# Kernel optimization log

Measured on AMD Instinct MI355X. Metric: run time of the kernel, lower is better.

## Reference

```python
import jax, jax.numpy as jnp
import numpy as np

ATOL = 1e-06
RTOL = 1e-06

def setup_inputs() -> dict:
    key = jax.random.key(0)
    ks = jax.random.split(key, 8)
    u = lambda k, shape: jax.random.uniform(k, shape, jnp.float32, -0.05, 0.05)
    return {
        "x": jax.random.normal(ks[0], (4096, 32, 32, 3), jnp.float32),
        "W_lstm": u(ks[1], (3, 16)),      # input kernel, gates [i,f,c,o]
        "U_lstm": u(ks[2], (4, 16)),      # recurrent kernel
        "dw_kernel": u(ks[3], (27, 27, 3, 5)),  # depthwise (kh,kw,in_c,mult)
        "pw_kernel": u(ks[4], (15, 4)),   # pointwise
        "conv_bias": u(ks[5], (4,)),
        "W_td": u(ks[6], (4096, 10)),
        "W_sc": u(ks[7], (4096, 10)),
    }

def _lstm_td(x, W, U):
    # TimeDistributed LSTM: x (B,32,32,3) -> treat axis1 as TD batch, axis2 as time
    B = x.shape[0]
    seq = x.reshape(B * 32, 32, 3)          # (N, T, F)
    xs = jnp.transpose(seq, (1, 0, 2))      # (T, N, F)
    N = seq.shape[0]
    h0 = jnp.zeros((N, 4), x.dtype)
    c0 = jnp.zeros((N, 4), x.dtype)

    def step(carry, xt):
        h, c = carry
        z = xt @ W + h @ U                  # (N, 16)
        zi, zf, zc, zo = jnp.split(z, 4, axis=-1)
        i = jax.nn.elu(zi)                  # recurrent_activation='elu'
        f = jax.nn.elu(zf)
        c = f * c + i * jax.nn.softmax(zc, axis=-1)  # activation='softmax'
        o = jax.nn.elu(zo)
        h = o * jax.nn.softmax(c, axis=-1)
        return (h, c), h

    _, hs = jax.lax.scan(step, (h0, c0), xs)        # (T, N, 4)
    return jnp.transpose(hs, (1, 0, 2)).reshape(B, 32, 32, 4)

def _sep_conv(x, dw_kernel, pw_kernel, conv_bias):
    # depthwise: Keras (kh,kw,C,M) -> lax HWIO grouped (kh,kw,1,C*M), channel-major order
    dw = dw_kernel.reshape(27, 27, 1, 15)
    y = jax.lax.conv_general_dilated(
        x, dw, window_strides=(1, 1), padding='SAME',
        feature_group_count=3,
        dimension_numbers=('NHWC', 'HWIO', 'NHWC'))   # (B,32,32,15)
    y = jnp.einsum('bhwc,cf->bhwf', y, pw_kernel) + conv_bias
    return jax.nn.sigmoid(y)                          # (B,32,32,4)

def reference(x, W_lstm, U_lstm, dw_kernel, pw_kernel, conv_bias, W_td, W_sc):
    B = x.shape[0]
    td = _lstm_td(x, W_lstm, U_lstm).reshape(B, -1) @ W_td   # (B,10)
    sc = _sep_conv(x, dw_kernel, pw_kernel, conv_bias).reshape(B, -1) @ W_sc
    diff = jnp.abs(td - sc)
    tol = ATOL + RTOL * jnp.abs(sc)
    return diff <= tol
```

## Files before the change

### kernel.cpp

```cpp
#include <hip/hip_runtime.h>
#include <math.h>

#define TD_OFF 0
#define WTDR_OFF 40960
#define SC_OFF 81920
#define BG_BYTE_OFF 524288

typedef __bf16 bf16x8 __attribute__((ext_vector_type(8)));
typedef float f32x16 __attribute__((ext_vector_type(16)));

union FragU { bf16x8 v; float4 f; };

__device__ __forceinline__ f32x16 mfma16(bf16x8 a, bf16x8 b, f32x16 c) {
    return __builtin_amdgcn_mfma_f32_32x32x16_bf16(a, b, c, 0, 0, 0);
}

__device__ __forceinline__ float eluf(float v) {
    return v > 0.f ? v : __expf(v) - 1.f;
}

__global__ __launch_bounds__(256) void prep(const float* __restrict__ dw,
                                            const float* __restrict__ pw,
                                            const float* __restrict__ Wtd,
                                            float* __restrict__ Wtdr,
                                            unsigned short* __restrict__ Bg) {
    int gid = blockIdx.x * 256 + threadIdx.x;
    if (gid < 40960) {
        int k = gid & 3;
        int r = gid >> 2;
        int row = r & 31; r >>= 5;
        int j = r % 10;
        int tt = r / 10;
        Wtdr[gid] = Wtd[(size_t)(row * 128 + tt * 4 + k) * 10 + j];
        return;
    }
    int g2 = gid - 40960;
    if (g2 >= 162 * 128) return;
    int n = g2 & 127;
    int s = g2 >> 7;
    int half = s & 1;
    int cd = s >> 1;
    int c = cd / 27, d = cd % 27;
    int w = n >> 2, f = n & 3;
    unsigned short* dsth = Bg + (size_t)s * 4096 + n * 16;
    unsigned short* dstl = dsth + 2048;
#pragma unroll
    for (int k = 0; k < 16; k++) {
        int xi = half * 16 + k;
        int dx = xi - w + 13;
        float v = 0.f;
        if (dx >= 0 && dx < 27) {
#pragma unroll
            for (int m = 0; m < 5; m++)
                v = fmaf(dw[((d * 27 + dx) * 3 + c) * 5 + m],
                         pw[(c * 5 + m) * 4 + f], v);
        }
        __bf16 h = (__bf16)v;
        __bf16 l = (__bf16)(v - (float)h);
        dsth[k] = __builtin_bit_cast(unsigned short, h);
        dstl[k] = __builtin_bit_cast(unsigned short, l);
    }
}

#define A_OFF 0
#define ZOFF 49152
#define SRED_OFF 49168
#define LDS_BYTES 49808

__global__ __launch_bounds__(256, 3) void fused(const float* __restrict__ x,
                                                const float* __restrict__ W,
                                                const float* __restrict__ U,
                                                const float* __restrict__ Wtdr,
                                                const unsigned short* __restrict__ Bg,
                                                const float* __restrict__ Wsc,
                                                const float* __restrict__ bias,
                                                float* __restrict__ td_out,
                                                float* __restrict__ sc_out) {
    __shared__ char LDS[LDS_BYTES] __attribute__((aligned(16)));
    int bx = blockIdx.x;
    int rem = bx % 3;
    int q = bx / 3;
    int t = threadIdx.x;

    if (rem == 2) {
        float rW[48], rU[64];
        const float4* W4 = (const float4*)W;
        const float4* U4 = (const float4*)U;
#pragma unroll
        for (int i = 0; i < 12; i++) {
            float4 qv = W4[i];
            rW[i * 4 + 0] = qv.x; rW[i * 4 + 1] = qv.y;
            rW[i * 4 + 2] = qv.z; rW[i * 4 + 3] = qv.w;
        }
#pragma unroll
        for (int i = 0; i < 16; i++) {
            float4 qv = U4[i];
            rU[i * 4 + 0] = qv.x; rU[i * 4 + 1] = qv.y;
            rU[i * 4 + 2] = qv.z; rU[i * 4 + 3] = qv.w;
        }

        int n = q * 256 + t;
        int row = n & 31;
        const float4* xp4 = (const float4*)(x + (size_t)n * 96);

        float h0 = 0, h1 = 0, h2 = 0, h3 = 0;
        float c0 = 0, c1 = 0, c2 = 0, c3 = 0;
        float acc[10];
#pragma unroll
        for (int j = 0; j < 10; j++) acc[j] = 0.f;

        for (int g = 0; g < 8; g++) {
            float4 q0 = xp4[g * 3 + 0], q1 = xp4[g * 3 + 1], q2 = xp4[g * 3 + 2];
            float xr[12] = {q0.x, q0.y, q0.z, q0.w, q1.x, q1.y,
                            q1.z, q1.w, q2.x, q2.y, q2.z, q2.w};
#pragma unroll
            for (int st = 0; st < 4; st++) {
                int tt = g * 4 + st;
                float x0 = xr[st * 3 + 0], x1 = xr[st * 3 + 1], x2 = xr[st * 3 + 2];
                float z[16];
#pragma unroll
                for (int k = 0; k < 16; k++)
                    z[k] = x0 * rW[k] + x1 * rW[16 + k] + x2 * rW[32 + k]
                         + h0 * rU[k] + h1 * rU[16 + k] + h2 * rU[32 + k] + h3 * rU[48 + k];

                float ig0 = eluf(z[0]),  ig1 = eluf(z[1]),  ig2 = eluf(z[2]),  ig3 = eluf(z[3]);
                float fg0 = eluf(z[4]),  fg1 = eluf(z[5]),  fg2 = eluf(z[6]),  fg3 = eluf(z[7]);
                float og0 = eluf(z[12]), og1 = eluf(z[13]), og2 = eluf(z[14]), og3 = eluf(z[15]);

                float zm = fmaxf(fmaxf(z[8], z[9]), fmaxf(z[10], z[11]));
                float e0 = __expf(z[8] - zm), e1 = __expf(z[9] - zm);
                float e2 = __expf(z[10] - zm), e3 = __expf(z[11] - zm);
                float inv = 1.f / (e0 + e1 + e2 + e3);
                c0 = fg0 * c0 + ig0 * (e0 * inv);
                c1 = fg1 * c1 + ig1 * (e1 * inv);
                c2 = fg2 * c2 + ig2 * (e2 * inv);
                c3 = fg3 * c3 + ig3 * (e3 * inv);

                float cm = fmaxf(fmaxf(c0, c1), fmaxf(c2, c3));
                float p0 = __expf(c0 - cm), p1 = __expf(c1 - cm);
                float p2 = __expf(c2 - cm), p3 = __expf(c3 - cm);
                float pinv = 1.f / (p0 + p1 + p2 + p3);
                h0 = og0 * (p0 * pinv); h1 = og1 * (p1 * pinv);
                h2 = og2 * (p2 * pinv); h3 = og3 * (p3 * pinv);

                const float4* wr4 = (const float4*)(Wtdr + (size_t)tt * 1280) + row;
#pragma unroll
                for (int j = 0; j < 10; j++) {
                    float4 qv = wr4[j * 32];
                    acc[j] += h0 * qv.x + h1 * qv.y + h2 * qv.z + h3 * qv.w;
                }
            }
        }

#pragma unroll
        for (int off = 16; off >= 1; off >>= 1) {
#pragma unroll
            for (int j = 0; j < 10; j++) acc[j] += __shfl_xor(acc[j], off, 64);
        }
        int lane = t & 63;
        if (lane == 0 || lane == 32) {
            int b = n >> 5;
#pragma unroll
            for (int j = 0; j < 10; j++) td_out[b * 10 + j] = acc[j];
        }
        return;
    }

    int ci = q * 2 + rem;
    int l = t & 63;
    int wv = t >> 6;
    int m = l & 31;
    int sub = l >> 5;

    const char* bbase = (const char*)Bg + (size_t)wv * 1024 + m * 32 + sub * 16;
    FragU bufA[2], bufB[2], bufC[2];
#define LOADB(sv, arr) { const char* p_ = bbase + (size_t)(sv) * 8192;       \
        arr[0].f = *(const float4*)(p_);                             \
        arr[1].f = *(const float4*)(p_ + 4096); }

    LOADB(0, bufA);
    LOADB(1, bufB);
    LOADB(2, bufC);

    const float* xb = x + (size_t)ci * 12288;
#pragma unroll
    for (int rep = 0; rep < 2; rep++) {
        int u = rep * 256 + t;
        int im = u >> 7;
        int woct = (u >> 5) & 3;
        int h = u & 31;
        const float4* src = (const float4*)(xb + im * 3072 + h * 96 + woct * 24);
        float xr[24];
#pragma unroll
        for (int i = 0; i < 6; i++) {
            float4 qv = src[i];
            xr[i * 4 + 0] = qv.x; xr[i * 4 + 1] = qv.y;
            xr[i * 4 + 2] = qv.z; xr[i * 4 + 3] = qv.w;
        }
#pragma unroll
        for (int c = 0; c < 3; c++) {
            FragU hiF, loF;
#pragma unroll
            for (int k = 0; k < 8; k++) {
                float v = xr[k * 3 + c];
                __bf16 hb = (__bf16)v;
                hiF.v[k] = hb;
                loF.v[k] = (__bf16)(v - (float)hb);
            }
            int rec = A_OFF + im * 12288 + (c * 8 + woct) * 512 + h * 16;
            *(float4*)(LDS + rec) = hiF.f;
            *(float4*)(LDS + rec + 2048) = loF.f;
        }
    }
    if (t < 4) *(float*)(LDS + ZOFF + t * 4) = 0.f;
    __syncthreads();

    f32x16 acc0 = {0,0,0,0,0,0,0,0,0,0,0,0,0,0,0,0};
    f32x16 acc1 = acc0, acc2 = acc0, acc3 = acc0;

    int c = 0, d = 0, half = 0;

#define CHUNK(USE, SNEXT) {                                                   \
    int rowIdx = m + d - 13;                                                  \
    bool valid = (unsigned)rowIdx < 32u;                                      \
    int a0 = A_OFF + (c * 8 + half * 2 + sub) * 512 + rowIdx * 16;            \
    FragU ah0, ah1, ah2, ah3, al0, al1, al2, al3;                             \
    ah0.f = *(const float4*)(LDS + (valid ? a0           : ZOFF));            \
    ah1.f = *(const float4*)(LDS + (valid ? a0 + 12288   : ZOFF));            \
    ah2.f = *(const float4*)(LDS + (valid ? a0 + 24576   : ZOFF));            \
    ah3.f = *(const float4*)(LDS + (valid ? a0 + 36864   : ZOFF));            \
    al0.f = *(const float4*)(LDS + (valid ? a0 + 2048    : ZOFF));            \
    al1.f = *(const float4*)(LDS + (valid ? a0 + 14336   : ZOFF));            \
    al2.f = *(const float4*)(LDS + (valid ? a0 + 26624   : ZOFF));            \
    al3.f = *(const float4*)(LDS + (valid ? a0 + 38912   : ZOFF));            \
    acc0 = mfma16(ah0.v, USE[0].v, acc0);                                     \
    acc1 = mfma16(ah1.v, USE[0].v, acc1);                                     \
    acc2 = mfma16(ah2.v, USE[0].v, acc2);                                     \
    acc3 = mfma16(ah3.v, USE[0].v, acc3);                                     \
    acc0 = mfma16(ah0.v, USE[1].v, acc0);                                     \
    acc1 = mfma16(ah1.v, USE[1].v, acc1);                                     \
    acc2 = mfma16(ah2.v, USE[1].v, acc2);                                     \
    acc3 = mfma16(ah3.v, USE[1].v, acc3);                                     \
    acc0 = mfma16(al0.v, USE[0].v, acc0);                                     \
    acc1 = mfma16(al1.v, USE[0].v, acc1);                                     \
    acc2 = mfma16(al2.v, USE[0].v, acc2);                                     \
    acc3 = mfma16(al3.v, USE[0].v, acc3);                                     \
    LOADB(SNEXT, USE);                                                        \
    half ^= 1;                                                                \
    if (!half) { d++; if (d == 27) { d = 0; c++; } }                          \
}

    for (int g = 0; g < 54; g++) {
        CHUNK(bufA, 3 * g + 3);
        CHUNK(bufB, 3 * g + 4);
        CHUNK(bufC, 3 * g + 5);
    }

    float b4[4];
#pragma unroll
    for (int i = 0; i < 4; i++) b4[i] = bias[i];

    float part[4][10];
#pragma unroll
    for (int i = 0; i < 4; i++)
#pragma unroll
        for (int j = 0; j < 10; j++) part[i][j] = 0.f;

    f32x16 accs[4] = {acc0, acc1, acc2, acc3};
    int ncol = wv * 32 + m;
    int wcol = ncol >> 2;
    int f = ncol & 3;
#pragma unroll
    for (int r = 0; r < 16; r++) {
        int h = (r & 3) + 8 * (r >> 2) + 4 * sub;
        const float* wr = Wsc + (size_t)((h * 32 + wcol) * 4 + f) * 10;
        float wreg[10];
#pragma unroll
        for (int j = 0; j < 10; j++) wreg[j] = wr[j];
#pragma unroll
        for (int im = 0; im < 4; im++) {
            float v = accs[im][r] + b4[f];
            float sg = 1.f / (1.f + expf(-v));
#pragma unroll
            for (int j = 0; j < 10; j++) part[im][j] = fmaf(sg, wreg[j], part[im][j]);
        }
    }

#pragma unroll
    for (int off = 32; off >= 1; off >>= 1) {
#pragma unroll
        for (int im = 0; im < 4; im++)
#pragma unroll
            for (int j = 0; j < 10; j++) part[im][j] += __shfl_xor(part[im][j], off, 64);
    }
    if (l == 0) {
        float* red = (float*)(LDS + SRED_OFF);
#pragma unroll
        for (int im = 0; im < 4; im++)
#pragma unroll
            for (int j = 0; j < 10; j++) red[(wv * 4 + im) * 10 + j] = part[im][j];
    }
    __syncthreads();
    if (t < 40) {
        int img = t / 10, j = t % 10;
        const float* red = (const float*)(LDS + SRED_OFF);
        float sv = red[(0 * 4 + img) * 10 + j] + red[(1 * 4 + img) * 10 + j]
                 + red[(2 * 4 + img) * 10 + j] + red[(3 * 4 + img) * 10 + j];
        sc_out[(ci * 4 + img) * 10 + j] = sv;
    }
}

__global__ __launch_bounds__(256) void cmp_k(const float* __restrict__ td,
                                             const float* __restrict__ sc,
                                             float* __restrict__ out) {
    int i = blockIdx.x * 256 + threadIdx.x;
    if (i < 40960) {
        float a = td[i];
        float s = sc[i];
        float tol = 1e-6f + 1e-6f * fabsf(s);
        out[i] = (fabsf(a - s) <= tol) ? 1.0f : 0.0f;
    }
}

extern "C" void kernel_launch(void* const* d_in, const int* in_sizes, int n_in,
                              void* d_out, int out_size, void* d_ws, size_t ws_size,
                              hipStream_t stream) {
    const float* x    = (const float*)d_in[0];
    const float* W    = (const float*)d_in[1];
    const float* U    = (const float*)d_in[2];
    const float* dw   = (const float*)d_in[3];
    const float* pw   = (const float*)d_in[4];
    const float* bias = (const float*)d_in[5];
    const float* Wtd  = (const float*)d_in[6];
    const float* Wsc  = (const float*)d_in[7];

    float* ws     = (float*)d_ws;
    float* td_acc = ws + TD_OFF;
    float* Wtdr   = ws + WTDR_OFF;
    float* sc_acc = ws + SC_OFF;
    unsigned short* Bg = (unsigned short*)((char*)d_ws + BG_BYTE_OFF);

    prep<<<241, 256, 0, stream>>>(dw, pw, Wtd, Wtdr, Bg);
    fused<<<1536, 256, 0, stream>>>(x, W, U, Wtdr, Bg, Wsc, bias, td_acc, sc_acc);
    cmp_k<<<160, 256, 0, stream>>>(td_acc, sc_acc, (float*)d_out);
}
```

Before: 361.7 us.

## Double-buffer LDS A-fragments across MFMA chunks and pack LSTM math into float2

The conv path now loads the next chunk's A fragments from LDS into registers while the current chunk's MFMAs run, using two register sets (aP/aQ), and the loop is unrolled by six so the ping-pong lines up with the three B buffers. This is meant to hide LDS latency behind matrix work, at the cost of more VGPRs, which could hurt occupancy at launch bounds of 3. The LSTM path stores gate weights and the TD accumulators as float2 vectors so the compiler can emit packed FP32 instructions. The epilogue sigmoid switches from expf to __expf, which is less accurate.

```diff
diff --git a/kernel.cpp b/kernel.cpp
--- a/kernel.cpp
+++ b/kernel.cpp
@@ -8,6 +8,7 @@
 
 typedef __bf16 bf16x8 __attribute__((ext_vector_type(8)));
 typedef float f32x16 __attribute__((ext_vector_type(16)));
+typedef float f32x2 __attribute__((ext_vector_type(2)));
 
 union FragU { bf16x8 v; float4 f; };
 
@@ -83,20 +84,18 @@
     int t = threadIdx.x;
 
     if (rem == 2) {
-        float rW[48], rU[64];
-        const float4* W4 = (const float4*)W;
-        const float4* U4 = (const float4*)U;
-#pragma unroll
-        for (int i = 0; i < 12; i++) {
-            float4 qv = W4[i];
-            rW[i * 4 + 0] = qv.x; rW[i * 4 + 1] = qv.y;
-            rW[i * 4 + 2] = qv.z; rW[i * 4 + 3] = qv.w;
-        }
-#pragma unroll
-        for (int i = 0; i < 16; i++) {
-            float4 qv = U4[i];
-            rU[i * 4 + 0] = qv.x; rU[i * 4 + 1] = qv.y;
-            rU[i * 4 + 2] = qv.z; rU[i * 4 + 3] = qv.w;
+        f32x2 sW0[8], sW1[8], sW2[8], sU0[8], sU1[8], sU2[8], sU3[8];
+        const f32x2* Wp = (const f32x2*)W;
+        const f32x2* Up = (const f32x2*)U;
+#pragma unroll
+        for (int k2 = 0; k2 < 8; k2++) {
+            sW0[k2] = Wp[k2];
+            sW1[k2] = Wp[8 + k2];
+            sW2[k2] = Wp[16 + k2];
+            sU0[k2] = Up[k2];
+            sU1[k2] = Up[8 + k2];
+            sU2[k2] = Up[16 + k2];
+            sU3[k2] = Up[24 + k2];
         }
 
         int n = q * 256 + t;
@@ -105,9 +104,9 @@
 
         float h0 = 0, h1 = 0, h2 = 0, h3 = 0;
         float c0 = 0, c1 = 0, c2 = 0, c3 = 0;
-        float acc[10];
-#pragma unroll
-        for (int j = 0; j < 10; j++) acc[j] = 0.f;
+        f32x2 pa2[10];
+#pragma unroll
+        for (int j = 0; j < 10; j++) pa2[j] = 0.f;
 
         for (int g = 0; g < 8; g++) {
             float4 q0 = xp4[g * 3 + 0], q1 = xp4[g * 3 + 1], q2 = xp4[g * 3 + 2];
@@ -117,19 +116,24 @@
             for (int st = 0; st < 4; st++) {
                 int tt = g * 4 + st;
                 float x0 = xr[st * 3 + 0], x1 = xr[st * 3 + 1], x2 = xr[st * 3 + 2];
-                float z[16];
-#pragma unroll
-                for (int k = 0; k < 16; k++)
-                    z[k] = x0 * rW[k] + x1 * rW[16 + k] + x2 * rW[32 + k]
-                         + h0 * rU[k] + h1 * rU[16 + k] + h2 * rU[32 + k] + h3 * rU[48 + k];
-
-                float ig0 = eluf(z[0]),  ig1 = eluf(z[1]),  ig2 = eluf(z[2]),  ig3 = eluf(z[3]);
-                float fg0 = eluf(z[4]),  fg1 = eluf(z[5]),  fg2 = eluf(z[6]),  fg3 = eluf(z[7]);
-                float og0 = eluf(z[12]), og1 = eluf(z[13]), og2 = eluf(z[14]), og3 = eluf(z[15]);
-
-                float zm = fmaxf(fmaxf(z[8], z[9]), fmaxf(z[10], z[11]));
-                float e0 = __expf(z[8] - zm), e1 = __expf(z[9] - zm);
-                float e2 = __expf(z[10] - zm), e3 = __expf(z[11] - zm);
+                f32x2 z2[8];
+#pragma unroll
+                for (int k2 = 0; k2 < 8; k2++)
+                    z2[k2] = sW0[k2] * x0 + sW1[k2] * x1 + sW2[k2] * x2
+                           + sU0[k2] * h0 + sU1[k2] * h1 + sU2[k2] * h2
+                           + sU3[k2] * h3;
+
+                float ig0 = eluf(z2[0][0]), ig1 = eluf(z2[0][1]);
+                float ig2 = eluf(z2[1][0]), ig3 = eluf(z2[1][1]);
+                float fg0 = eluf(z2[2][0]), fg1 = eluf(z2[2][1]);
+                float fg2 = eluf(z2[3][0]), fg3 = eluf(z2[3][1]);
+                float og0 = eluf(z2[6][0]), og1 = eluf(z2[6][1]);
+                float og2 = eluf(z2[7][0]), og3 = eluf(z2[7][1]);
+
+                float zc0 = z2[4][0], zc1 = z2[4][1], zc2 = z2[5][0], zc3 = z2[5][1];
+                float zm = fmaxf(fmaxf(zc0, zc1), fmaxf(zc2, zc3));
+                float e0 = __expf(zc0 - zm), e1 = __expf(zc1 - zm);
+                float e2 = __expf(zc2 - zm), e3 = __expf(zc3 - zm);
                 float inv = 1.f / (e0 + e1 + e2 + e3);
                 c0 = fg0 * c0 + ig0 * (e0 * inv);
                 c1 = fg1 * c1 + ig1 * (e1 * inv);
@@ -143,15 +147,17 @@
                 h0 = og0 * (p0 * pinv); h1 = og1 * (p1 * pinv);
                 h2 = og2 * (p2 * pinv); h3 = og3 * (p3 * pinv);
 
-                const float4* wr4 = (const float4*)(Wtdr + (size_t)tt * 1280) + row;
-#pragma unroll
-                for (int j = 0; j < 10; j++) {
-                    float4 qv = wr4[j * 32];
-                    acc[j] += h0 * qv.x + h1 * qv.y + h2 * qv.z + h3 * qv.w;
-                }
+                const f32x2* wr2 = (const f32x2*)(Wtdr + (size_t)tt * 1280) + row * 2;
+                f32x2 h01 = {h0, h1}, h23 = {h2, h3};
+#pragma unroll
+                for (int j = 0; j < 10; j++)
+                    pa2[j] += h01 * wr2[j * 64] + h23 * wr2[j * 64 + 1];
             }
         }
 
+        float acc[10];
+#pragma unroll
+        for (int j = 0; j < 10; j++) acc[j] = pa2[j][0] + pa2[j][1];
 #pragma unroll
         for (int off = 16; off >= 1; off >>= 1) {
 #pragma unroll
@@ -198,16 +204,16 @@
             xr[i * 4 + 2] = qv.z; xr[i * 4 + 3] = qv.w;
         }
 #pragma unroll
-        for (int c = 0; c < 3; c++) {
+        for (int cc = 0; cc < 3; cc++) {
             FragU hiF, loF;
 #pragma unroll
             for (int k = 0; k < 8; k++) {
-                float v = xr[k * 3 + c];
+                float v = xr[k * 3 + cc];
                 __bf16 hb = (__bf16)v;
                 hiF.v[k] = hb;
                 loF.v[k] = (__bf16)(v - (float)hb);
             }
-            int rec = A_OFF + im * 12288 + (c * 8 + woct) * 512 + h * 16;
+            int rec = A_OFF + im * 12288 + (cc * 8 + woct) * 512 + h * 16;
             *(float4*)(LDS + rec) = hiF.f;
             *(float4*)(LDS + rec + 2048) = loF.f;
         }
@@ -218,42 +224,50 @@
     f32x16 acc0 = {0,0,0,0,0,0,0,0,0,0,0,0,0,0,0,0};
     f32x16 acc1 = acc0, acc2 = acc0, acc3 = acc0;
 
+    FragU aP[8], aQ[8];
     int c = 0, d = 0, half = 0;
 
-#define CHUNK(USE, SNEXT) {                                                   \
+#define ISSUE_A(dst) {                                                        \
     int rowIdx = m + d - 13;                                                  \
-    bool valid = (unsigned)rowIdx < 32u;                                      \
+    bool valid = ((unsigned)rowIdx < 32u) && (c < 3);                         \
     int a0 = A_OFF + (c * 8 + half * 2 + sub) * 512 + rowIdx * 16;            \
-    FragU ah0, ah1, ah2, ah3, al0, al1, al2, al3;                             \
-    ah0.f = *(const float4*)(LDS + (valid ? a0           : ZOFF));            \
-    ah1.f = *(const float4*)(LDS + (valid ? a0 + 12288   : ZOFF));            \
-    ah2.f = *(const float4*)(LDS + (valid ? a0 + 24576   : ZOFF));            \
-    ah3.f = *(const float4*)(LDS + (valid ? a0 + 36864   : ZOFF));            \
-    al0.f = *(const float4*)(LDS + (valid ? a0 + 2048    : ZOFF));            \
-    al1.f = *(const float4*)(LDS + (valid ? a0 + 14336   : ZOFF));            \
-    al2.f = *(const float4*)(LDS + (valid ? a0 + 26624   : ZOFF));            \
-    al3.f = *(const float4*)(LDS + (valid ? a0 + 38912   : ZOFF));            \
-    acc0 = mfma16(ah0.v, USE[0].v, acc0);                                     \
-    acc1 = mfma16(ah1.v, USE[0].v, acc1);                                     \
-    acc2 = mfma16(ah2.v, USE[0].v, acc2);                                     \
-    acc3 = mfma16(ah3.v, USE[0].v, acc3);                                     \
-    acc0 = mfma16(ah0.v, USE[1].v, acc0);                                     \
-    acc1 = mfma16(ah1.v, USE[1].v, acc1);                                     \
-    acc2 = mfma16(ah2.v, USE[1].v, acc2);                                     \
-    acc3 = mfma16(ah3.v, USE[1].v, acc3);                                     \
-    acc0 = mfma16(al0.v, USE[0].v, acc0);                                     \
-    acc1 = mfma16(al1.v, USE[0].v, acc1);                                     \
-    acc2 = mfma16(al2.v, USE[0].v, acc2);                                     \
-    acc3 = mfma16(al3.v, USE[0].v, acc3);                                     \
-    LOADB(SNEXT, USE);                                                        \
+    dst[0].f = *(const float4*)(LDS + (valid ? a0           : ZOFF));         \
+    dst[1].f = *(const float4*)(LDS + (valid ? a0 + 12288   : ZOFF));         \
+    dst[2].f = *(const float4*)(LDS + (valid ? a0 + 24576   : ZOFF));         \
+    dst[3].f = *(const float4*)(LDS + (valid ? a0 + 36864   : ZOFF));         \
+    dst[4].f = *(const float4*)(LDS + (valid ? a0 + 2048    : ZOFF));         \
+    dst[5].f = *(const float4*)(LDS + (valid ? a0 + 14336   : ZOFF));         \
+    dst[6].f = *(const float4*)(LDS + (valid ? a0 + 26624   : ZOFF));         \
+    dst[7].f = *(const float4*)(LDS + (valid ? a0 + 38912   : ZOFF));         \
     half ^= 1;                                                                \
     if (!half) { d++; if (d == 27) { d = 0; c++; } }                          \
 }
 
-    for (int g = 0; g < 54; g++) {
-        CHUNK(bufA, 3 * g + 3);
-        CHUNK(bufB, 3 * g + 4);
-        CHUNK(bufC, 3 * g + 5);
+#define CHUNK(USE, ACUR, ANXT, SNEXT) {                                       \
+    ISSUE_A(ANXT);                                                            \
+    acc0 = mfma16(ACUR[0].v, USE[0].v, acc0);                                 \
+    acc1 = mfma16(ACUR[1].v, USE[0].v, acc1);                                 \
+    acc2 = mfma16(ACUR[2].v, USE[0].v, acc2);                                 \
+    acc3 = mfma16(ACUR[3].v, USE[0].v, acc3);                                 \
+    acc0 = mfma16(ACUR[0].v, USE[1].v, acc0);                                 \
+    acc1 = mfma16(ACUR[1].v, USE[1].v, acc1);                                 \
+    acc2 = mfma16(ACUR[2].v, USE[1].v, acc2);                                 \
+    acc3 = mfma16(ACUR[3].v, USE[1].v, acc3);                                 \
+    acc0 = mfma16(ACUR[4].v, USE[0].v, acc0);                                 \
+    acc1 = mfma16(ACUR[5].v, USE[0].v, acc1);                                 \
+    acc2 = mfma16(ACUR[6].v, USE[0].v, acc2);                                 \
+    acc3 = mfma16(ACUR[7].v, USE[0].v, acc3);                                 \
+    LOADB(SNEXT, USE);                                                        \
+}
+
+    ISSUE_A(aP);
+    for (int g = 0; g < 27; g++) {
+        CHUNK(bufA, aP, aQ, 6 * g + 3);
+        CHUNK(bufB, aQ, aP, 6 * g + 4);
+        CHUNK(bufC, aP, aQ, 6 * g + 5);
+        CHUNK(bufA, aQ, aP, 6 * g + 6);
+        CHUNK(bufB, aP, aQ, 6 * g + 7);
+        CHUNK(bufC, aQ, aP, 6 * g + 8);
     }
 
     float b4[4];
@@ -280,7 +294,7 @@
 #pragma unroll
         for (int im = 0; im < 4; im++) {
             float v = accs[im][r] + b4[f];
-            float sg = 1.f / (1.f + expf(-v));
+            float sg = 1.f / (1.f + __expf(-v));
 #pragma unroll
             for (int j = 0; j < 10; j++) part[im][j] = fmaf(sg, wreg[j], part[im][j]);
         }
```

After: 364.5 us, median of 2. Within noise of the previous version (+0.8%).
